# Kernel optimization log

Measured on AMD Instinct MI355X. Metric: run time of the kernel, lower is better.

Reference implementation:

```python
import jax, jax.numpy as jnp
import numpy as np
from jax import lax

HID = 128  # hidden_dim
K = 2      # kernel (must be 2 for the torch slice arithmetic to be shape-consistent)


def skew(x):
    # x: (B,C,H,W) -> (B,C,H,2W-1), row r shifted right by r
    B, C, H, W = x.shape
    rows = jnp.arange(H)[:, None]
    cols = jnp.arange(W)[None, :] + rows
    y = jnp.zeros((B, C, H, 2 * W - 1), x.dtype)
    return y.at[:, :, rows, cols].set(x)


def unskew(x):
    B, C, H, Wp = x.shape
    W = (Wp + 1) // 2
    rows = jnp.arange(H)[:, None]
    cols = jnp.arange(W)[None, :] + rows
    return x[:, :, rows, cols]


def setup_inputs() -> dict:
    key = jax.random.key(0)
    k1, k2, k3 = jax.random.split(key, 3)
    Cin = 128
    x = jax.random.normal(k1, (8, Cin, 64, 64), jnp.float32)
    w_is = jax.random.normal(k2, (4 * HID, Cin), jnp.float32) * 0.05   # 1x1 conv weight
    b_is = jnp.zeros((4 * HID,), jnp.float32)
    w_ss = jax.random.normal(k3, (4 * HID, HID, K, 1), jnp.float32) * 0.05  # (k,1) conv weight
    b_ss = jnp.zeros((4 * HID,), jnp.float32)
    return {"x": x, "w_is": w_is, "b_is": b_is, "w_ss": w_ss, "b_ss": b_ss}


def reference(x, w_is, b_is, w_ss, b_ss):
    B, Cin, H, W = x.shape
    hid, k = HID, K
    xs = skew(x)  # (B,Cin,H,2W-1)
    # input-to-state: 1x1 conv (mask B on 1x1 kernel == plain 1x1 conv)
    z_is = jnp.einsum('bchw,oc->bohw', xs, w_is) + b_is[None, :, None, None]
    steps = z_is.transpose(3, 0, 1, 2)  # (2W-1, B, 4hid, H)

    h0 = jnp.zeros((B, hid, H), x.dtype)
    c0 = jnp.zeros((B, hid, H), x.dtype)

    def step(carry, z_t):
        h, c = carry  # (B,hid,H)
        # state-to-state (k,1) conv along H, padding k//2, then drop last k-1 rows
        hs = lax.conv_general_dilated(h[..., None], w_ss, (1, 1),
                                      [(k // 2, k // 2), (0, 0)],
                                      dimension_numbers=('NCHW', 'OIHW', 'NCHW'))
        hs = hs[:, :, :-(k - 1), 0] + b_ss[None, :, None]  # (B,4hid,H)
        z = z_t + hs
        i = jax.nn.sigmoid(z[:, :hid])
        f = jax.nn.sigmoid(z[:, hid:2 * hid])
        o = jax.nn.sigmoid(z[:, 2 * hid:3 * hid])
        g = jnp.tanh(z[:, 3 * hid:])
        c = f * c + i * g
        h = o * jnp.tanh(c)
        return (h, c), h

    _, hs_all = lax.scan(step, (h0, c0), steps)  # (2W-1,B,hid,H)
    out = hs_all.transpose(1, 2, 3, 0)  # (B,hid,H,2W-1)
    return unskew(out)  # (B,hid,H,W)
```

## Files before the change

kernel.cpp:

```cpp
#include <hip/hip_runtime.h>
#include <hip/hip_fp16.h>
#include <math.h>


#define HID 128
#define BB 8
#define HH 64
#define WW 64
#define TT 127

#define NPREP 1022

typedef _Float16 v8h __attribute__((ext_vector_type(8)));
typedef float v4f __attribute__((ext_vector_type(4)));

#define SENT64 0xFFFFFFFFFFFFFFFFULL

__device__ __forceinline__ float fsig(float x) {
  float e = __builtin_amdgcn_exp2f(x * -1.44269504f);
  return __builtin_amdgcn_rcpf(1.f + e);
}
__device__ __forceinline__ float ftanh_(float x) {
  float e = __builtin_amdgcn_exp2f(x * 2.88539009f);
  return __builtin_fmaf(-2.f, __builtin_amdgcn_rcpf(1.f + e), 1.f);
}

__global__ __launch_bounds__(256) void prep_zpre(
    const float* __restrict__ x, const float* __restrict__ w_is,
    const float* __restrict__ b_is, const float* __restrict__ b_ss,
    const float* __restrict__ w_ss, _Float16* __restrict__ wp,
    __half* __restrict__ zph, unsigned long long* __restrict__ hx) {
  const int bid = blockIdx.x;
  const int tid = threadIdx.x;

  __shared__ _Float16 xt[64][136];

  if (bid < NPREP) {
    int idx = bid * 256 + tid;
    if (idx < 131072) {
      int j = idx & 7;
      int L = (idx >> 3) & 63;
      int kt = (idx >> 9) & 7;
      int mt = idx >> 12;
      int O = mt * 16 + (L & 15);
      int k = kt * 32 + ((L >> 4) & 3) * 8 + j;
      float v = (k < 128) ? w_ss[(size_t)O * 256 + k * 2]
                          : w_ss[(size_t)O * 256 + (k - 128) * 2 + 1];
      wp[idx] = (_Float16)v;
    } else if (idx < 131584) {
      int idx2 = idx - 131072;
      int g = (idx2 >> 2) & 3;
      int u = (idx2 >> 4) * 4 + (idx2 & 3);
      int O = g * 128 + u;
      zph[(size_t)BB * HH * WW * 512 + idx2] = __float2half(b_is[O] + b_ss[O]);
    } else {
      int j = idx - 131584;
      uint4 s;
      s.x = 0xFFFFFFFFu;
      s.y = 0xFFFFFFFFu;
      s.z = 0xFFFFFFFFu;
      s.w = 0xFFFFFFFFu;
      ((uint4*)hx)[j] = s;
    }
    return;
  }

  const int zb = bid - NPREP;
  const int b = zb >> 6;
  const int r = zb & 63;
  const int wv = tid >> 6;
  const int L = tid & 63;
  const int quad = L >> 4;
  const int l15 = L & 15;

  {
    const int cw = tid >> 4;
    const int w4 = (tid & 15) * 4;
#pragma unroll
    for (int p = 0; p < 8; p++) {
      int c = p * 16 + cw;
      float4 v = *(const float4*)&x[(((size_t)b * 128 + c) * HH + r) * WW + w4];
      xt[w4 + 0][c] = (_Float16)v.x;
      xt[w4 + 1][c] = (_Float16)v.y;
      xt[w4 + 2][c] = (_Float16)v.z;
      xt[w4 + 3][c] = (_Float16)v.w;
    }
  }

  v8h wfr[8][4];
  float4 bv[8];
#pragma unroll
  for (int m = 0; m < 8; m++) {
    const int mt = 8 * wv + m;
    const int O = mt * 16 + l15;
#pragma unroll
    for (int kt = 0; kt < 4; kt++) {
      const float* p = w_is + (size_t)O * 128 + kt * 32 + quad * 8;
      float4 a = *(const float4*)p;
      float4 b2 = *(const float4*)(p + 4);
      v8h f;
      f[0] = (_Float16)a.x;
      f[1] = (_Float16)a.y;
      f[2] = (_Float16)a.z;
      f[3] = (_Float16)a.w;
      f[4] = (_Float16)b2.x;
      f[5] = (_Float16)b2.y;
      f[6] = (_Float16)b2.z;
      f[7] = (_Float16)b2.w;
      wfr[m][kt] = f;
    }
    const int O4 = mt * 16 + quad * 4;
    float4 bi = *(const float4*)&b_is[O4];
    float4 bs4 = *(const float4*)&b_ss[O4];
    bv[m] = make_float4(bi.x + bs4.x, bi.y + bs4.y, bi.z + bs4.z, bi.w + bs4.w);
  }

  __syncthreads();

#pragma unroll
  for (int nt = 0; nt < 4; nt++) {
    v8h bf[4];
#pragma unroll
    for (int kt = 0; kt < 4; kt++)
      bf[kt] = *(const v8h*)&xt[nt * 16 + l15][kt * 32 + quad * 8];
    const size_t pos = ((size_t)b * HH + r) * WW + nt * 16 + l15;
#pragma unroll
    for (int m = 0; m < 8; m++) {
      v4f acc = (v4f){0.f, 0.f, 0.f, 0.f};
#pragma unroll
      for (int kt = 0; kt < 4; kt++)
        acc = __builtin_amdgcn_mfma_f32_16x16x32_f16(wfr[m][kt], bf[kt], acc,
                                                     0, 0, 0);
      const int mt = 8 * wv + m;
      __half2 lo = __floats2half2_rn(acc[0] + bv[m].x, acc[1] + bv[m].y);
      __half2 hi = __floats2half2_rn(acc[2] + bv[m].z, acc[3] + bv[m].w);
      uint2 pk;
      pk.x = *(unsigned*)&lo;
      pk.y = *(unsigned*)&hi;
      *(uint2*)&zph[pos * 512 + (m * 4 + quad) * 16 + wv * 4] = pk;
    }
  }
}

#define HROW 136

#define STEP_BARRIER()                                   \
  do {                                                   \
    asm volatile("s_waitcnt lgkmcnt(0)" ::: "memory");   \
    __builtin_amdgcn_s_barrier();                        \
    asm volatile("" ::: "memory");                       \
  } while (0)

#define STEP_BODY(T, RB)                                                       \
  do {                                                                         \
           \
    v8h bfr[4];                                                                \
    _Pragma("unroll") for (int kt = 0; kt < 4; kt++)                           \
        bfr[kt] = *(const v8h*)&h_lds[RB][(rl * 2 + bl) * HROW + kt * 32 +     \
                                          quad * 8];                           \
         \
    v4f zi[4];                                                                 \
    _Pragma("unroll") for (int g = 0; g < 4; g++)                              \
        _Pragma("unroll") for (int i = 0; i < 4; i++)                          \
        zi[g][i] = __half2float(zu.h[g * 4 + i]);                              \
         \
    {                                                                          \
      const uint4* p = (const uint4*)(((unsigned)wn < WW) ? zcur : zbias);     \
      zu.q[0] = p[0];                                                          \
      zu.q[1] = p[1];                                                          \
      wn++;                                                                    \
      zcur += 512;                                                             \
    }                                                                          \
          \
    v4f acc0[4], acc1[4];                                                      \
    _Pragma("unroll") for (int g = 0; g < 4; g++) {                            \
      acc0[g] = (v4f){0.f, 0.f, 0.f, 0.f};                                     \
      acc1[g] = zi[g];                                                         \
    }                                                                          \
    _Pragma("unroll") for (int kt = 0; kt < 4; kt++) {                         \
      _Pragma("unroll") for (int g = 0; g < 4; g++)                            \
          acc0[g] = __builtin_amdgcn_mfma_f32_16x16x32_f16(                    \
              wfrag[g][kt], bfr[kt], acc0[g], 0, 0, 0);                        \
    }                                                                          \
    _Pragma("unroll") for (int kt = 0; kt < 4; kt++) {                         \
      v8h bf1 = *(const v8h*)&h_lds[RB][((rl + 1) * 2 + bl) * HROW + kt * 32 + \
                                        quad * 8];                             \
      _Pragma("unroll") for (int g = 0; g < 4; g++)                            \
          acc1[g] = __builtin_amdgcn_mfma_f32_16x16x32_f16(                    \
              wfrag[g][4 + kt], bf1, acc1[g], 0, 0, 0);                        \
    }                                                                          \
          \
    unsigned long long pend = 0ull;                                            \
    if (is_cons)                                                               \
      pend = __hip_atomic_load(ca, __ATOMIC_RELAXED,                           \
                               __HIP_MEMORY_SCOPE_AGENT);                      \
                        \
    const int w = (T)-r;                                                       \
    const bool inband = ((unsigned)w < WW);                                    \
    float hv[4];                                                               \
    _Pragma("unroll") for (int rg2 = 0; rg2 < 4; rg2++) {                      \
      float z0 = acc0[0][rg2] + acc1[0][rg2];                                  \
      float z1 = acc0[1][rg2] + acc1[1][rg2];                                  \
      float z2 = acc0[2][rg2] + acc1[2][rg2];                                  \
      float z3 = acc0[3][rg2] + acc1[3][rg2];                                  \
      float iv = fsig(z0);                                                     \
      float fv = fsig(z1);                                                     \
      float ov = fsig(z2);                                                     \
      float gv = ftanh_(z3);                                                   \
      c[rg2] = fv * c[rg2] + iv * gv;                                          \
      hv[rg2] = ov * ftanh_(c[rg2]);                                           \
    }                                                                          \
                       \
    __half2 plo = __floats2half2_rn(hv[0], hv[1]);                             \
    __half2 phi = __floats2half2_rn(hv[2], hv[3]);                             \
    {                                                                          \
      uint2 pk;                                                                \
      pk.x = *(unsigned*)&plo;                                                 \
      pk.y = *(unsigned*)&phi;                                                 \
      *(uint2*)&h_lds[(RB) ^ 1][((rl + 1) * 2 + bl) * HROW + uq0] = pk;        \
    }                                                                          \
              \
    if (rgr < 7 && l15 >= 14) {                                                \
      unsigned long long pk =                                                  \
          ((unsigned long long)*(unsigned*)&phi << 32) | *(unsigned*)&plo;     \
      __hip_atomic_store(pa, pk, __ATOMIC_RELAXED, __HIP_MEMORY_SCOPE_AGENT);  \
    }                                                                          \
    pa += 2048;                                                                \
             \
    _Pragma("unroll") for (int rg2 = 0; rg2 < 4; rg2++) {                      \
      outb[rg2].x = outb[rg2].y;                                               \
      outb[rg2].y = outb[rg2].z;                                               \
      outb[rg2].z = outb[rg2].w;                                               \
      outb[rg2].w = hv[rg2];                                                   \
    }                                                                          \
    if (inband && (w & 3) == 3) {                                              \
      *(float4*)op0 = outb[0];                                                 \
      *(float4*)op1 = outb[1];                                                 \
      *(float4*)op2 = outb[2];                                                 \
      *(float4*)op3 = outb[3];                                                 \
      op0 += 4;                                                                \
      op1 += 4;                                                                \
      op2 += 4;                                                                \
      op3 += 4;                                                                \
    }                                                                          \
                   \
    if (is_cons) {                                                             \
      while (__ballot(pend == SENT64) != 0ull) {                               \
        __builtin_amdgcn_s_sleep(1);                                           \
        pend = __hip_atomic_load(ca, __ATOMIC_RELAXED,                         \
                                 __HIP_MEMORY_SCOPE_AGENT);                    \
      }                                                                        \
      *(unsigned long long*)&h_lds[(RB) ^ 1][(0 * 2 + ebl) * HROW + eu] =      \
          pend;                                                                \
    }                                                                          \
    ca += 2048;                                                                \
    STEP_BARRIER();                                                            \
  } while (0)

__global__ __launch_bounds__(512, 1) void lstm_mfma(
    const __half* __restrict__ zph, const _Float16* __restrict__ wp,
    unsigned long long* __restrict__ hx,
    float* __restrict__ out) {
  const int blk = blockIdx.x;
  const int rgr = blk >> 2;
  const int bg = blk & 3;
  const int R0 = rgr * 8;
  const int tid = threadIdx.x;
  const int wv = tid >> 6;
  const int L = tid & 63;
  const int quad = L >> 4;
  const int l15 = L & 15;
  const int rl = l15 >> 1;
  const int bl = l15 & 1;
  const int b = bg * 2 + bl;
  const int r = R0 + rl;
  const int uq0 = 16 * wv + quad * 4;
  const int zoff = (4 * wv + quad) * 16;

  __shared__ _Float16 h_lds[2][9 * 2 * HROW];
  for (int i = tid; i < (2 * 9 * 2 * HROW) / 2; i += 512)
    ((unsigned*)h_lds)[i] = 0u;

  v8h wfrag[4][8];
  {
    const v8h* wp8 = (const v8h*)wp;
#pragma unroll
    for (int g = 0; g < 4; g++)
#pragma unroll
      for (int kt = 0; kt < 8; kt++)
        wfrag[g][kt] = wp8[((size_t)((8 * g + wv) * 8 + kt)) * 64 + L];
  }

  float c[4] = {0.f, 0.f, 0.f, 0.f};
  float4 outb[4];
#pragma unroll
  for (int i = 0; i < 4; i++) outb[i] = make_float4(0.f, 0.f, 0.f, 0.f);

  const int ebl = L >> 5;
  const int eu = (L & 31) * 4;
  const int exp_idx = bl * 32 + 4 * wv + quad;

  const bool is_cons = (wv == 0) && (rgr > 0);

  const __half* zpp = zph + ((size_t)b * HH + r) * WW * 512 + zoff;
  const __half* zbias = zph + (size_t)BB * HH * WW * 512 + zoff;
  const unsigned long long* ca =
      hx + (((size_t)(rgr > 0 ? rgr - 1 : 0) * 4 + bg) * 64 + L);
  unsigned long long* pa = hx + (((size_t)rgr * 4 + bg) * 64 + exp_idx);
  float* op0 = out + (((size_t)b * HID + uq0 + 0) * HH + r) * WW;
  float* op1 = out + (((size_t)b * HID + uq0 + 1) * HH + r) * WW;
  float* op2 = out + (((size_t)b * HID + uq0 + 2) * HH + r) * WW;
  float* op3 = out + (((size_t)b * HID + uq0 + 3) * HH + r) * WW;

  union ZU {
    uint4 q[2];
    __half h[16];
  } zu;
  {
    const uint4* p0 = (const uint4*)((r == 0) ? zpp : zbias);
    zu.q[0] = p0[0];
    zu.q[1] = p0[1];
  }
  int wn = 1 - r;
  const __half* zcur = zpp + (ptrdiff_t)wn * 512;

  __syncthreads();

  for (int t = 0; t < TT - 1; t += 2) {
    STEP_BODY(t, 0);
    STEP_BODY(t + 1, 1);
  }
  STEP_BODY(TT - 1, 0);
}

__global__ __launch_bounds__(256) void transpose_x(const float* __restrict__ x,
                                                   float* __restrict__ xT) {
  int b = blockIdx.x >> 6;
  int r = blockIdx.x & 63;
  __shared__ float tile[32][65];
  for (int cc = 0; cc < 4; cc++) {
    int cl = threadIdx.x >> 6;
    int w = threadIdx.x & 63;
#pragma unroll
    for (int k = 0; k < 8; k++) {
      int c_loc = k * 4 + cl;
      int c = cc * 32 + c_loc;
      tile[c_loc][w] = x[(((size_t)b * 128 + c) * HH + r) * WW + w];
    }
    __syncthreads();
    int cs = threadIdx.x & 31;
    int wp = threadIdx.x >> 5;
#pragma unroll
    for (int k = 0; k < 8; k++) {
      int w2 = wp * 8 + k;
      xT[(((size_t)b * HH + r) * WW + w2) * 128 + cc * 32 + cs] = tile[cs][w2];
    }
    __syncthreads();
  }
}

__global__ __launch_bounds__(256) void step_kernel(
    const float* __restrict__ x, const float* __restrict__ xT, int use_xT,
    const float* __restrict__ w_is, const float* __restrict__ b_is,
    const float* __restrict__ w_ss, const float* __restrict__ b_ss,
    const float* __restrict__ h_prev, float* __restrict__ h_next,
    float* __restrict__ c_state, float* __restrict__ out, int t) {
  const int rg = blockIdx.x;
  const int q = blockIdx.y;
  const int r0 = rg * 2;
  const int tid = threadIdx.x;
  const int o_loc = tid & 63;
  const int k4 = tid >> 6;
  const int g_ = o_loc >> 4;
  const int u_ = o_loc & 15;
  const int O = g_ * 128 + q * 16 + u_;
  const int i0 = k4 * 32;

  __shared__ __align__(16) float h_in[3][BB][HID];
  __shared__ float zred[16][4][65];

  for (int idx = tid; idx < 3 * BB * HID; idx += 256) {
    int row_sel = idx >> 10;
    int rem = idx & 1023;
    int b = rem >> 7;
    int u = rem & 127;
    int rr = r0 - 1 + row_sel;
    h_in[row_sel][b][u] = (rr >= 0) ? h_prev[((size_t)b * HH + rr) * HID + u] : 0.0f;
  }

  float wr0[32], wr1[32], wz[32];
  {
    const float4* wss4 = (const float4*)(w_ss + ((size_t)O * 128 + i0) * 2);
#pragma unroll
    for (int j = 0; j < 16; j++) {
      float4 v = wss4[j];
      wr0[2 * j] = v.x;
      wr1[2 * j] = v.y;
      wr0[2 * j + 1] = v.z;
      wr1[2 * j + 1] = v.w;
    }
    const float4* wis4 = (const float4*)(w_is + (size_t)O * 128 + i0);
#pragma unroll
    for (int j = 0; j < 8; j++) {
      float4 v = wis4[j];
      wz[4 * j] = v.x;
      wz[4 * j + 1] = v.y;
      wz[4 * j + 2] = v.z;
      wz[4 * j + 3] = v.w;
    }
  }

  __syncthreads();

  float acc[2][BB];
#pragma unroll
  for (int rl = 0; rl < 2; rl++)
#pragma unroll
    for (int b = 0; b < BB; b++) acc[rl][b] = 0.0f;

#pragma unroll
  for (int jb = 0; jb < 8; jb++) {
    int ib = i0 + jb * 4;
#pragma unroll
    for (int b = 0; b < BB; b++) {
      const float4 hm4 = *(const float4*)&h_in[0][b][ib];
      const float4 hc4 = *(const float4*)&h_in[1][b][ib];
      const float4 hp4 = *(const float4*)&h_in[2][b][ib];
      const float* hm = (const float*)&hm4;
      const float* hc = (const float*)&hc4;
      const float* hq = (const float*)&hp4;
#pragma unroll
      for (int jj = 0; jj < 4; jj++) {
        float w0v = wr0[jb * 4 + jj];
        float w1v = wr1[jb * 4 + jj];
        acc[0][b] += w0v * hm[jj] + w1v * hc[jj];
        acc[1][b] += w0v * hc[jj] + w1v * hq[jj];
      }
    }
  }

#pragma unroll
  for (int rl = 0; rl < 2; rl++) {
    int rr = r0 + rl;
    int wcol = t - rr;
    if (wcol >= 0 && wcol < WW) {
      if (use_xT) {
        for (int b = 0; b < BB; b++) {
          const float4* xp =
              (const float4*)(xT + (((size_t)b * HH + rr) * WW + wcol) * 128 + i0);
#pragma unroll
          for (int j = 0; j < 8; j++) {
            float4 v = xp[j];
            acc[rl][b] += wz[4 * j] * v.x + wz[4 * j + 1] * v.y +
                          wz[4 * j + 2] * v.z + wz[4 * j + 3] * v.w;
          }
        }
      } else {
        for (int b = 0; b < BB; b++) {
          const float* xb = x + (((size_t)b * 128 + i0) * HH + rr) * WW + wcol;
#pragma unroll
          for (int j = 0; j < 32; j++) {
            acc[rl][b] += wz[j] * xb[(size_t)j * HH * WW];
          }
        }
      }
    }
  }

#pragma unroll
  for (int rl = 0; rl < 2; rl++)
#pragma unroll
    for (int b = 0; b < BB; b++) zred[rl * 8 + b][k4][o_loc] = acc[rl][b];
  __syncthreads();

  {
    int u = tid >> 4;
    int cell = tid & 15;
    int rl = cell >> 3;
    int b = cell & 7;
    int rr = r0 + rl;
    float z[4];
#pragma unroll
    for (int gg = 0; gg < 4; gg++) {
      int ol = gg * 16 + u;
      float s = zred[cell][0][ol] + zred[cell][1][ol] + zred[cell][2][ol] +
                zred[cell][3][ol];
      int Og = gg * 128 + q * 16 + u;
      z[gg] = s + b_is[Og] + b_ss[Og];
    }
    float iv = 1.0f / (1.0f + expf(-z[0]));
    float fv = 1.0f / (1.0f + expf(-z[1]));
    float ov = 1.0f / (1.0f + expf(-z[2]));
    float gv = tanhf(z[3]);
    int U = q * 16 + u;
    size_t sidx = ((size_t)b * HH + rr) * HID + U;
    float cv = c_state[sidx];
    float cn = fv * cv + iv * gv;
    c_state[sidx] = cn;
    float hn = ov * tanhf(cn);
    h_next[sidx] = hn;
    int wcol = t - rr;
    if (wcol >= 0 && wcol < WW) {
      out[(((size_t)b * HID + U) * HH + rr) * WW + wcol] = hn;
    }
  }
}

extern "C" void kernel_launch(void* const* d_in, const int* in_sizes, int n_in,
                              void* d_out, int out_size, void* d_ws,
                              size_t ws_size, hipStream_t stream) {
  const float* x = (const float*)d_in[0];
  const float* w_is = (const float*)d_in[1];
  const float* b_is = (const float*)d_in[2];
  const float* w_ss = (const float*)d_in[3];
  const float* b_ss = (const float*)d_in[4];
  float* outp = (float*)d_out;

  const size_t zph_bytes = ((size_t)BB * HH * WW * 512 + 512) * 2;
  const size_t wp_bytes = (size_t)512 * 256 * 2;
  const size_t hx_bytes = (size_t)TT * 8 * 4 * 64 * 8;
  const size_t need = zph_bytes + wp_bytes + hx_bytes;

  char* ws = (char*)d_ws;
  if (ws_size >= need) {
    __half* zph = (__half*)ws;
    _Float16* wpp = (_Float16*)(ws + zph_bytes);
    unsigned long long* hx =
        (unsigned long long*)(ws + zph_bytes + wp_bytes);

    prep_zpre<<<dim3(NPREP + 512), 256, 0, stream>>>(x, w_is, b_is, b_ss,
                                                     w_ss, wpp, zph, hx);
    lstm_mfma<<<dim3(32), 512, 0, stream>>>(zph, wpp, hx, outp);
  } else {
    const size_t xT_elems = (size_t)BB * HH * WW * 128;
    const size_t st_elems = (size_t)BB * HH * HID;
    const size_t need_xT = (xT_elems + 3 * st_elems) * sizeof(float);
    float* wsf = (float*)d_ws;
    float* xT = nullptr;
    float* st;
    int use_xT = 0;
    if (ws_size >= need_xT) {
      use_xT = 1;
      xT = wsf;
      st = wsf + xT_elems;
    } else {
      st = wsf;
    }
    float* h0 = st;
    float* h1 = st + st_elems;
    float* cb = st + 2 * st_elems;
    hipMemsetAsync(st, 0, 3 * st_elems * sizeof(float), stream);
    if (use_xT) transpose_x<<<dim3(BB * HH), 256, 0, stream>>>(x, xT);
    for (int t = 0; t < TT; t++) {
      float* hp = (t & 1) ? h1 : h0;
      float* hn = (t & 1) ? h0 : h1;
      step_kernel<<<dim3(32, 8), 256, 0, stream>>>(x, xT, use_xT, w_is, b_is,
                                                   w_ss, b_ss, hp, hn, cb, outp,
                                                   t);
    }
  }
}
```

Before: 290.9 us.

## Fuse input-to-state projection into recurrent LSTM kernel blocks

Moves the 1x1-conv input projection (x times w_is, plus biases) out of the large prep grid and into the 32-block recurrent kernel. Each block computes z_pre only for the 16 (batch, row) pairs it will consume before the scan begins. The prep kernel now only packs w_ss, writes the bias row and initialises the flags. This removes the separate 512-block GEMM phase and its round trip through global memory between launches. The cost is that the GEMM now runs on only 32 blocks with serial 16-iteration loops, which may underuse the GPU.

Result: slower. 359.5 us (+23.6%).

```diff
diff --git a/kernel.cpp b/kernel.cpp
--- a/kernel.cpp
+++ b/kernel.cpp
@@ -11,6 +11,8 @@
 
 #define NPREP 1022
 
+#define HROW 136
+
 typedef _Float16 v8h __attribute__((ext_vector_type(8)));
 typedef float v4f __attribute__((ext_vector_type(4)));
 
@@ -25,124 +27,35 @@
   return __builtin_fmaf(-2.f, __builtin_amdgcn_rcpf(1.f + e), 1.f);
 }
 
-__global__ __launch_bounds__(256) void prep_zpre(
-    const float* __restrict__ x, const float* __restrict__ w_is,
-    const float* __restrict__ b_is, const float* __restrict__ b_ss,
-    const float* __restrict__ w_ss, _Float16* __restrict__ wp,
+__global__ __launch_bounds__(256) void prep_k(
+    const float* __restrict__ w_ss, const float* __restrict__ b_is,
+    const float* __restrict__ b_ss, _Float16* __restrict__ wp,
     __half* __restrict__ zph, unsigned long long* __restrict__ hx) {
-  const int bid = blockIdx.x;
-  const int tid = threadIdx.x;
-
-  __shared__ _Float16 xt[64][136];
-
-  if (bid < NPREP) {
-    int idx = bid * 256 + tid;
-    if (idx < 131072) {
-      int j = idx & 7;
-      int L = (idx >> 3) & 63;
-      int kt = (idx >> 9) & 7;
-      int mt = idx >> 12;
-      int O = mt * 16 + (L & 15);
-      int k = kt * 32 + ((L >> 4) & 3) * 8 + j;
-      float v = (k < 128) ? w_ss[(size_t)O * 256 + k * 2]
-                          : w_ss[(size_t)O * 256 + (k - 128) * 2 + 1];
-      wp[idx] = (_Float16)v;
-    } else if (idx < 131584) {
-      int idx2 = idx - 131072;
-      int g = (idx2 >> 2) & 3;
-      int u = (idx2 >> 4) * 4 + (idx2 & 3);
-      int O = g * 128 + u;
-      zph[(size_t)BB * HH * WW * 512 + idx2] = __float2half(b_is[O] + b_ss[O]);
-    } else {
-      int j = idx - 131584;
-      uint4 s;
-      s.x = 0xFFFFFFFFu;
-      s.y = 0xFFFFFFFFu;
-      s.z = 0xFFFFFFFFu;
-      s.w = 0xFFFFFFFFu;
-      ((uint4*)hx)[j] = s;
-    }
-    return;
-  }
-
-  const int zb = bid - NPREP;
-  const int b = zb >> 6;
-  const int r = zb & 63;
-  const int wv = tid >> 6;
-  const int L = tid & 63;
-  const int quad = L >> 4;
-  const int l15 = L & 15;
-
-  {
-    const int cw = tid >> 4;
-    const int w4 = (tid & 15) * 4;
-#pragma unroll
-    for (int p = 0; p < 8; p++) {
-      int c = p * 16 + cw;
-      float4 v = *(const float4*)&x[(((size_t)b * 128 + c) * HH + r) * WW + w4];
-      xt[w4 + 0][c] = (_Float16)v.x;
-      xt[w4 + 1][c] = (_Float16)v.y;
-      xt[w4 + 2][c] = (_Float16)v.z;
-      xt[w4 + 3][c] = (_Float16)v.w;
-    }
-  }
-
-  v8h wfr[8][4];
-  float4 bv[8];
-#pragma unroll
-  for (int m = 0; m < 8; m++) {
-    const int mt = 8 * wv + m;
-    const int O = mt * 16 + l15;
-#pragma unroll
-    for (int kt = 0; kt < 4; kt++) {
-      const float* p = w_is + (size_t)O * 128 + kt * 32 + quad * 8;
-      float4 a = *(const float4*)p;
-      float4 b2 = *(const float4*)(p + 4);
-      v8h f;
-      f[0] = (_Float16)a.x;
-      f[1] = (_Float16)a.y;
-      f[2] = (_Float16)a.z;
-      f[3] = (_Float16)a.w;
-      f[4] = (_Float16)b2.x;
-      f[5] = (_Float16)b2.y;
-      f[6] = (_Float16)b2.z;
-      f[7] = (_Float16)b2.w;
-      wfr[m][kt] = f;
-    }
-    const int O4 = mt * 16 + quad * 4;
-    float4 bi = *(const float4*)&b_is[O4];
-    float4 bs4 = *(const float4*)&b_ss[O4];
-    bv[m] = make_float4(bi.x + bs4.x, bi.y + bs4.y, bi.z + bs4.z, bi.w + bs4.w);
-  }
-
-  __syncthreads();
-
-#pragma unroll
-  for (int nt = 0; nt < 4; nt++) {
-    v8h bf[4];
-#pragma unroll
-    for (int kt = 0; kt < 4; kt++)
-      bf[kt] = *(const v8h*)&xt[nt * 16 + l15][kt * 32 + quad * 8];
-    const size_t pos = ((size_t)b * HH + r) * WW + nt * 16 + l15;
-#pragma unroll
-    for (int m = 0; m < 8; m++) {
-      v4f acc = (v4f){0.f, 0.f, 0.f, 0.f};
-#pragma unroll
-      for (int kt = 0; kt < 4; kt++)
-        acc = __builtin_amdgcn_mfma_f32_16x16x32_f16(wfr[m][kt], bf[kt], acc,
-                                                     0, 0, 0);
-      const int mt = 8 * wv + m;
-      __half2 lo = __floats2half2_rn(acc[0] + bv[m].x, acc[1] + bv[m].y);
-      __half2 hi = __floats2half2_rn(acc[2] + bv[m].z, acc[3] + bv[m].w);
-      uint2 pk;
-      pk.x = *(unsigned*)&lo;
-      pk.y = *(unsigned*)&hi;
-      *(uint2*)&zph[pos * 512 + (m * 4 + quad) * 16 + wv * 4] = pk;
-    }
-  }
-}
-
-#define HROW 136
+  int idx = blockIdx.x * 256 + threadIdx.x;
+  if (idx < 131072) {
+    int j = idx & 7;
+    int L = (idx >> 3) & 63;
+    int kt = (idx >> 9) & 7;
+    int mt = idx >> 12;
+    int O = mt * 16 + (L & 15);
+    int k = kt * 32 + ((L >> 4) & 3) * 8 + j;
+    float v = (k < 128) ? w_ss[(size_t)O * 256 + k * 2]
+                        : w_ss[(size_t)O * 256 + (k - 128) * 2 + 1];
+    wp[idx] = (_Float16)v;
+  } else if (idx < 131584) {
+    int idx2 = idx - 131072;
+    int g = (idx2 >> 2) & 3;
+    int u = (idx2 >> 4) * 4 + (idx2 & 3);
+    int O = g * 128 + u;
+    zph[(size_t)BB * HH * WW * 512 + idx2] = __float2half(b_is[O] + b_ss[O]);
+  } else {
+    int j = idx - 131584;
+    uint4 s;
+    s.x = 0xFFFFFFFFu; s.y = 0xFFFFFFFFu;
+    s.z = 0xFFFFFFFFu; s.w = 0xFFFFFFFFu;
+    ((uint4*)hx)[j] = s;
+  }
+}
 
 #define STEP_BARRIER()                                   \
   do {                                                   \
@@ -150,6 +63,8 @@
     __builtin_amdgcn_s_barrier();                        \
     asm volatile("" ::: "memory");                       \
   } while (0)
+
+#define HPLD(p) __hip_atomic_load((p), __ATOMIC_RELAXED, __HIP_MEMORY_SCOPE_AGENT)
 
 #define STEP_BODY(T, RB)                                                       \
   do {                                                                         \
@@ -158,7 +73,7 @@
     _Pragma("unroll") for (int kt = 0; kt < 4; kt++)                           \
         bfr[kt] = *(const v8h*)&h_lds[RB][(rl * 2 + bl) * HROW + kt * 32 +     \
                                           quad * 8];                           \
-         \
+                               \
     v4f zi[4];                                                                 \
     _Pragma("unroll") for (int g = 0; g < 4; g++)                              \
         _Pragma("unroll") for (int i = 0; i < 4; i++)                          \
@@ -189,11 +104,9 @@
           acc1[g] = __builtin_amdgcn_mfma_f32_16x16x32_f16(                    \
               wfrag[g][4 + kt], bf1, acc1[g], 0, 0, 0);                        \
     }                                                                          \
-          \
+         \
     unsigned long long pend = 0ull;                                            \
-    if (is_cons)                                                               \
-      pend = __hip_atomic_load(ca, __ATOMIC_RELAXED,                           \
-                               __HIP_MEMORY_SCOPE_AGENT);                      \
+    if (is_cons) pend = HPLD(ca);                                              \
                         \
     const int w = (T)-r;                                                       \
     const bool inband = ((unsigned)w < WW);                                    \
@@ -223,9 +136,10 @@
     if (rgr < 7 && l15 >= 14) {                                                \
       unsigned long long pk =                                                  \
           ((unsigned long long)*(unsigned*)&phi << 32) | *(unsigned*)&plo;     \
-      __hip_atomic_store(pa, pk, __ATOMIC_RELAXED, __HIP_MEMORY_SCOPE_AGENT);  \
-    }                                                                          \
-    pa += 2048;                                                                \
+      __hip_atomic_store(pa_hx, pk, __ATOMIC_RELAXED,                          \
+                         __HIP_MEMORY_SCOPE_AGENT);                            \
+    }                                                                          \
+    pa_hx += 2048;                                                             \
              \
     _Pragma("unroll") for (int rg2 = 0; rg2 < 4; rg2++) {                      \
       outb[rg2].x = outb[rg2].y;                                               \
@@ -238,17 +152,13 @@
       *(float4*)op1 = outb[1];                                                 \
       *(float4*)op2 = outb[2];                                                 \
       *(float4*)op3 = outb[3];                                                 \
-      op0 += 4;                                                                \
-      op1 += 4;                                                                \
-      op2 += 4;                                                                \
-      op3 += 4;                                                                \
-    }                                                                          \
-                   \
+      op0 += 4; op1 += 4; op2 += 4; op3 += 4;                                  \
+    }                                                                          \
+                          \
     if (is_cons) {                                                             \
       while (__ballot(pend == SENT64) != 0ull) {                               \
         __builtin_amdgcn_s_sleep(1);                                           \
-        pend = __hip_atomic_load(ca, __ATOMIC_RELAXED,                         \
-                                 __HIP_MEMORY_SCOPE_AGENT);                    \
+        pend = HPLD(ca);                                                       \
       }                                                                        \
       *(unsigned long long*)&h_lds[(RB) ^ 1][(0 * 2 + ebl) * HROW + eu] =      \
           pend;                                                                \
@@ -258,9 +168,11 @@
   } while (0)
 
 __global__ __launch_bounds__(512, 1) void lstm_mfma(
-    const __half* __restrict__ zph, const _Float16* __restrict__ wp,
+    const __half* __restrict__ zphc, const _Float16* __restrict__ wp,
     unsigned long long* __restrict__ hx,
-    float* __restrict__ out) {
+    float* __restrict__ out, const float* __restrict__ x,
+    const float* __restrict__ w_is, const float* __restrict__ b_is,
+    const float* __restrict__ b_ss, __half* __restrict__ zphw) {
   const int blk = blockIdx.x;
   const int rgr = blk >> 2;
   const int bg = blk & 3;
@@ -278,8 +190,84 @@
   const int zoff = (4 * wv + quad) * 16;
 
   __shared__ _Float16 h_lds[2][9 * 2 * HROW];
+  __shared__ _Float16 xt[64][136];
   for (int i = tid; i < (2 * 9 * 2 * HROW) / 2; i += 512)
     ((unsigned*)h_lds)[i] = 0u;
+
+  {
+    v8h wfr[4][4];
+    float4 bvv[4];
+#pragma unroll
+    for (int m = 0; m < 4; m++) {
+      const int mt = 4 * wv + m;
+      const int O = mt * 16 + l15;
+#pragma unroll
+      for (int kt = 0; kt < 4; kt++) {
+        const float* p = w_is + (size_t)O * 128 + kt * 32 + quad * 8;
+        float4 a = *(const float4*)p;
+        float4 b2 = *(const float4*)(p + 4);
+        v8h f;
+        f[0] = (_Float16)a.x;  f[1] = (_Float16)a.y;
+        f[2] = (_Float16)a.z;  f[3] = (_Float16)a.w;
+        f[4] = (_Float16)b2.x; f[5] = (_Float16)b2.y;
+        f[6] = (_Float16)b2.z; f[7] = (_Float16)b2.w;
+        wfr[m][kt] = f;
+      }
+      const int O4 = mt * 16 + quad * 4;
+      float4 bi = *(const float4*)&b_is[O4];
+      float4 bs4 = *(const float4*)&b_ss[O4];
+      bvv[m] = make_float4(bi.x + bs4.x, bi.y + bs4.y, bi.z + bs4.z,
+                           bi.w + bs4.w);
+    }
+
+    for (int tt = 0; tt < 16; tt++) {
+      const int b2 = bg * 2 + (tt & 1);
+      const int r2 = R0 + (tt >> 1);
+      __syncthreads();
+      {
+        const int cw = tid >> 4;
+        const int w4 = (tid & 15) * 4;
+#pragma unroll
+        for (int p = 0; p < 4; p++) {
+          int cc = p * 32 + cw;
+          float4 v =
+              *(const float4*)&x[(((size_t)b2 * 128 + cc) * HH + r2) * WW + w4];
+          xt[w4 + 0][cc] = (_Float16)v.x;
+          xt[w4 + 1][cc] = (_Float16)v.y;
+          xt[w4 + 2][cc] = (_Float16)v.z;
+          xt[w4 + 3][cc] = (_Float16)v.w;
+        }
+      }
+      __syncthreads();
+#pragma unroll
+      for (int nt = 0; nt < 4; nt++) {
+        v8h bf[4];
+#pragma unroll
+        for (int kt = 0; kt < 4; kt++)
+          bf[kt] = *(const v8h*)&xt[nt * 16 + l15][kt * 32 + quad * 8];
+        const size_t pos = ((size_t)b2 * HH + r2) * WW + nt * 16 + l15;
+#pragma unroll
+        for (int m = 0; m < 4; m++) {
+          v4f acc = (v4f){0.f, 0.f, 0.f, 0.f};
+#pragma unroll
+          for (int kt = 0; kt < 4; kt++)
+            acc = __builtin_amdgcn_mfma_f32_16x16x32_f16(wfr[m][kt], bf[kt],
+                                                         acc, 0, 0, 0);
+          const int mt = 4 * wv + m;
+          __half2 lo = __floats2half2_rn(acc[0] + bvv[m].x, acc[1] + bvv[m].y);
+          __half2 hi = __floats2half2_rn(acc[2] + bvv[m].z, acc[3] + bvv[m].w);
+          uint2 pk;
+          pk.x = *(unsigned*)&lo;
+          pk.y = *(unsigned*)&hi;
+          *(uint2*)&zphw[pos * 512 + ((mt & 7) * 4 + quad) * 16 +
+                         (mt >> 3) * 4] = pk;
+        }
+      }
+    }
+    asm volatile("s_waitcnt vmcnt(0)" ::: "memory");
+    __syncthreads();
+  }
+  const __half* zph = zphc;
 
   v8h wfrag[4][8];
   {
@@ -306,7 +294,7 @@
   const __half* zbias = zph + (size_t)BB * HH * WW * 512 + zoff;
   const unsigned long long* ca =
       hx + (((size_t)(rgr > 0 ? rgr - 1 : 0) * 4 + bg) * 64 + L);
-  unsigned long long* pa = hx + (((size_t)rgr * 4 + bg) * 64 + exp_idx);
+  unsigned long long* pa_hx = hx + (((size_t)rgr * 4 + bg) * 64 + exp_idx);
   float* op0 = out + (((size_t)b * HID + uq0 + 0) * HH + r) * WW;
   float* op1 = out + (((size_t)b * HID + uq0 + 1) * HH + r) * WW;
   float* op2 = out + (((size_t)b * HID + uq0 + 2) * HH + r) * WW;
@@ -528,9 +516,9 @@
     unsigned long long* hx =
         (unsigned long long*)(ws + zph_bytes + wp_bytes);
 
-    prep_zpre<<<dim3(NPREP + 512), 256, 0, stream>>>(x, w_is, b_is, b_ss,
-                                                     w_ss, wpp, zph, hx);
-    lstm_mfma<<<dim3(32), 512, 0, stream>>>(zph, wpp, hx, outp);
+    prep_k<<<dim3(NPREP), 256, 0, stream>>>(w_ss, b_is, b_ss, wpp, zph, hx);
+    lstm_mfma<<<dim3(32), 512, 0, stream>>>(zph, wpp, hx, outp, x, w_is,
+                                            b_is, b_ss, zph);
   } else {
     const size_t xT_elems = (size_t)BB * HH * WW * 128;
     const size_t st_elems = (size_t)BB * HH * HID;
```
